# Kernel optimization log

Hardware: AMD Instinct MI355X
Metric: run time of the kernel (lower is better)

## Reference

```python
import jax, jax.numpy as jnp
import numpy as np

N_STARS = 2048   # n_stars
BATCH = 256      # query positions per call
PF = 28          # poly_features = (d_max+1)(d_max+2)/2, d_max=6
NGE = 512        # n_graph_elems
GF = 32          # graph_features
OPD = 256        # opd_dim


def setup_inputs() -> dict:
    key = jax.random.key(0)
    ks = jax.random.split(key, 8)
    # observed star positions in the FoV (x_lims/y_lims = [0,1000])
    obs_pos = jax.random.uniform(ks[0], (N_STARS, 2), jnp.float32, 0.0, 1000.0)
    # query positions are exact rows of obs_pos (required by the exact-match index search)
    idx = jax.random.randint(ks[1], (BATCH,), 0, N_STARS)
    positions = obs_pos[idx]
    poly_dic = jax.random.normal(ks[2], (N_STARS, PF), jnp.float32)
    graph_dic = jax.random.normal(ks[3], (N_STARS, NGE), jnp.float32)
    # alpha matrices: identity(-padded) init as in init_vars, plus small noise
    alpha_poly = jnp.eye(PF, dtype=jnp.float32) + 0.01 * jax.random.normal(ks[4], (PF, PF), jnp.float32)
    alpha_graph = (jnp.eye(NGE, GF, dtype=jnp.float32)
                   + 0.01 * jax.random.normal(ks[5], (NGE, GF), jnp.float32))
    # S features: random uniform in [-1e-3, 1e-3] as in init_vars
    S_poly = jax.random.uniform(ks[6], (PF, OPD, OPD), jnp.float32, -0.001, 0.001)
    S_graph = jax.random.uniform(ks[7], (GF, OPD, OPD), jnp.float32, -0.001, 0.001)
    return {
        'positions': positions, 'obs_pos': obs_pos,
        'poly_dic': poly_dic, 'graph_dic': graph_dic,
        'alpha_poly': alpha_poly, 'alpha_graph': alpha_graph,
        'S_poly': S_poly, 'S_graph': S_graph,
    }


def _calc_indices(positions, obs_pos):
    # Faithful to tf.where(tf.equal(obs_pos, pos))[0, 0]: first True entry (row-major)
    # of the elementwise equality over (n_stars, 2); its row index is taken.
    eq = positions[:, None, :] == obs_pos[None, :, :]          # (B, N, 2) bool
    flat_first = jnp.argmax(eq.reshape(eq.shape[0], -1), axis=1)  # first True, flat index
    return flat_first // 2                                      # row index in obs_pos


def reference(positions, obs_pos, poly_dic, graph_dic, alpha_poly, alpha_graph, S_poly, S_graph):
    indices = _calc_indices(positions, obs_pos)                 # (B,) int
    # polynomial part: gather -> matmul -> tensordot with OPD modes
    batch_poly = jnp.take(poly_dic, indices, axis=0)            # (B, PF)
    interm_poly = batch_poly @ alpha_poly                       # (B, PF)
    contrib_poly = jnp.einsum('bp,pij->bij', interm_poly, S_poly)  # (B, OPD, OPD)
    # graph part
    batch_graph = jnp.take(graph_dic, indices, axis=0)          # (B, NGE)
    interm_graph = batch_graph @ alpha_graph                    # (B, GF)
    contrib_graph = jnp.einsum('bg,gij->bij', interm_graph, S_graph)
    return contrib_poly + contrib_graph
```

## Files before the change

### kernel.cpp

```cpp
#include <hip/hip_runtime.h>

#define NSTARS 2048
#define BATCH  256
#define PF     28
#define NGE    512
#define GF     32
#define OPD2   65536
#define KTOT   (PF + GF)
#define TM     16

typedef float f32x4 __attribute__((ext_vector_type(4)));

__global__ __launch_bounds__(256) void prep_kernel(
    const float* __restrict__ positions,  const float* __restrict__ obs_pos,
    const float* __restrict__ poly_dic,   const float* __restrict__ graph_dic,
    const float* __restrict__ alpha_poly, const float* __restrict__ alpha_graph,
    float* __restrict__ Wt)
{
    const int b = blockIdx.x;
    const int t = threadIdx.x;

    const float p0 = positions[2 * b];
    const float p1 = positions[2 * b + 1];

    int cand = 0x7fffffff;
    #pragma unroll
    for (int i = 0; i < NSTARS / 256; ++i) {
        const int n = t + i * 256;
        const float o0 = obs_pos[2 * n];
        const float o1 = obs_pos[2 * n + 1];
        if (o0 == p0 || o1 == p1) cand = min(cand, n);
    }
    __shared__ int smin[256];
    smin[t] = cand;
    __syncthreads();
    for (int s = 128; s > 0; s >>= 1) {
        if (t < s) smin[t] = min(smin[t], smin[t + s]);
        __syncthreads();
    }
    int idx = smin[0];
    if (idx == 0x7fffffff) idx = 0;

    if (t < PF) {
        float acc = 0.f;
        #pragma unroll
        for (int p = 0; p < PF; ++p)
            acc += poly_dic[idx * PF + p] * alpha_poly[p * PF + t];
        Wt[t * BATCH + b] = acc;
    }

    __shared__ float psum[8][GF];
    {
        const int g = t & 31;
        const int r = t >> 5;
        float acc = 0.f;
        const int e0 = r * (NGE / 8);
        for (int e = e0; e < e0 + NGE / 8; ++e)
            acc += graph_dic[idx * NGE + e] * alpha_graph[e * GF + g];
        psum[r][g] = acc;
    }
    __syncthreads();
    if (t < GF) {
        float acc = 0.f;
        #pragma unroll
        for (int r = 0; r < 8; ++r) acc += psum[r][t];
        Wt[(PF + t) * BATCH + b] = acc;
    }
}

__global__ __launch_bounds__(256) void main_kernel(
    const float* __restrict__ S_poly, const float* __restrict__ S_graph,
    const float* __restrict__ Wt, float* __restrict__ out)
{
    const int t    = threadIdx.x;
    const int id   = blockIdx.x;
    const int xcd  = id & 7;
    const int slot = id >> 3;
    const int xb   = xcd * 8 + (slot & 7);
    const int yb   = slot >> 3;

    const int ij = xb * 1024 + t * 4;
    const int b0 = yb * TM;

    f32x4 acc[TM];
    #pragma unroll
    for (int b = 0; b < TM; ++b) acc[b] = (f32x4)(0.f);

    const float* __restrict__ wp = Wt + b0;

    #pragma unroll 8
    for (int k = 0; k < PF; ++k) {
        const f32x4 s = *reinterpret_cast<const f32x4*>(
            S_poly + (size_t)k * OPD2 + ij);
        #pragma unroll
        for (int b = 0; b < TM; ++b) {
            const float w = wp[k * BATCH + b];
            acc[b].x = fmaf(w, s.x, acc[b].x);
            acc[b].y = fmaf(w, s.y, acc[b].y);
            acc[b].z = fmaf(w, s.z, acc[b].z);
            acc[b].w = fmaf(w, s.w, acc[b].w);
        }
    }
    #pragma unroll 8
    for (int k = 0; k < GF; ++k) {
        const f32x4 s = *reinterpret_cast<const f32x4*>(
            S_graph + (size_t)k * OPD2 + ij);
        #pragma unroll
        for (int b = 0; b < TM; ++b) {
            const float w = wp[(PF + k) * BATCH + b];
            acc[b].x = fmaf(w, s.x, acc[b].x);
            acc[b].y = fmaf(w, s.y, acc[b].y);
            acc[b].z = fmaf(w, s.z, acc[b].z);
            acc[b].w = fmaf(w, s.w, acc[b].w);
        }
    }

    #pragma unroll
    for (int b = 0; b < TM; ++b) {
        __builtin_nontemporal_store(
            acc[b],
            reinterpret_cast<f32x4*>(out + (size_t)(b0 + b) * OPD2 + ij));
    }
}

extern "C" void kernel_launch(void* const* d_in, const int* in_sizes, int n_in,
                              void* d_out, int out_size, void* d_ws, size_t ws_size,
                              hipStream_t stream) {
    const float* positions   = (const float*)d_in[0];
    const float* obs_pos     = (const float*)d_in[1];
    const float* poly_dic    = (const float*)d_in[2];
    const float* graph_dic   = (const float*)d_in[3];
    const float* alpha_poly  = (const float*)d_in[4];
    const float* alpha_graph = (const float*)d_in[5];
    const float* S_poly      = (const float*)d_in[6];
    const float* S_graph     = (const float*)d_in[7];
    float* out = (float*)d_out;

    float* Wt = (float*)d_ws;

    prep_kernel<<<BATCH, 256, 0, stream>>>(positions, obs_pos, poly_dic,
                                           graph_dic, alpha_poly, alpha_graph,
                                           Wt);

    main_kernel<<<1024, 256, 0, stream>>>(S_poly, S_graph, Wt, out);
}
```

Measured before the change: 131.0 us.

## Double-buffer S tiles in LDS via async global_load_lds

The main kernel now stages the S coefficient tiles (four k-slices at a time) into a double-buffered shared-memory array using direct global-to-LDS loads. The next stage is prefetched while FMAs run on the current one. The aim is to hide global load latency behind compute. In exchange it adds a block barrier and a full vmcnt wait every stage, and the w loads from global, which are also vector memory ops, get serialized by those waits.

```diff
diff --git a/kernel.cpp b/kernel.cpp
--- a/kernel.cpp
+++ b/kernel.cpp
@@ -8,6 +8,8 @@
 #define OPD2   65536
 #define KTOT   (PF + GF)
 #define TM     16
+#define KB     4
+#define NT     (KTOT / KB)
 
 typedef float f32x4 __attribute__((ext_vector_type(4)));
 
@@ -72,6 +74,8 @@
     const float* __restrict__ S_poly, const float* __restrict__ S_graph,
     const float* __restrict__ Wt, float* __restrict__ out)
 {
+    __shared__ float sbuf[2][KB][1024];
+
     const int t    = threadIdx.x;
     const int id   = blockIdx.x;
     const int xcd  = id & 7;
@@ -82,37 +86,54 @@
     const int ij = xb * 1024 + t * 4;
     const int b0 = yb * TM;
 
+    const float* __restrict__ wp = Wt + b0;
+
     f32x4 acc[TM];
     #pragma unroll
     for (int b = 0; b < TM; ++b) acc[b] = (f32x4)(0.f);
 
-    const float* __restrict__ wp = Wt + b0;
+    const int wbase = (t >> 6) << 8;
 
-    #pragma unroll 8
-    for (int k = 0; k < PF; ++k) {
-        const f32x4 s = *reinterpret_cast<const f32x4*>(
-            S_poly + (size_t)k * OPD2 + ij);
+    auto stage = [&](int T, int d) {
+        const int kb = T * KB;
+        const float* base = (T < PF / KB)
+            ? (S_poly  + (size_t)kb * OPD2)
+            : (S_graph + (size_t)(kb - PF) * OPD2);
+        const float* src = base + xb * 1024 + t * 4;
         #pragma unroll
-        for (int b = 0; b < TM; ++b) {
-            const float w = wp[k * BATCH + b];
-            acc[b].x = fmaf(w, s.x, acc[b].x);
-            acc[b].y = fmaf(w, s.y, acc[b].y);
-            acc[b].z = fmaf(w, s.z, acc[b].z);
-            acc[b].w = fmaf(w, s.w, acc[b].w);
+        for (int kk = 0; kk < KB; ++kk) {
+            __builtin_amdgcn_global_load_lds(
+                (const __attribute__((address_space(1))) uint32_t*)(src + (size_t)kk * OPD2),
+                (__attribute__((address_space(3))) uint32_t*)&sbuf[d][kk][wbase],
+                16, 0, 0);
         }
-    }
-    #pragma unroll 8
-    for (int k = 0; k < GF; ++k) {
-        const f32x4 s = *reinterpret_cast<const f32x4*>(
-            S_graph + (size_t)k * OPD2 + ij);
+    };
+
+    stage(0, 0);
+    asm volatile("s_waitcnt vmcnt(0)" ::: "memory");
+    __syncthreads();
+
+    int cur = 0;
+    for (int T = 0; T < NT; ++T) {
+        if (T + 1 < NT) stage(T + 1, cur ^ 1);
+
+        const int kb = T * KB;
         #pragma unroll
-        for (int b = 0; b < TM; ++b) {
-            const float w = wp[(PF + k) * BATCH + b];
-            acc[b].x = fmaf(w, s.x, acc[b].x);
-            acc[b].y = fmaf(w, s.y, acc[b].y);
-            acc[b].z = fmaf(w, s.z, acc[b].z);
-            acc[b].w = fmaf(w, s.w, acc[b].w);
+        for (int kk = 0; kk < KB; ++kk) {
+            const f32x4 s = *reinterpret_cast<const f32x4*>(&sbuf[cur][kk][t * 4]);
+            #pragma unroll
+            for (int b = 0; b < TM; ++b) {
+                const float w = wp[(kb + kk) * BATCH + b];
+                acc[b].x = fmaf(w, s.x, acc[b].x);
+                acc[b].y = fmaf(w, s.y, acc[b].y);
+                acc[b].z = fmaf(w, s.z, acc[b].z);
+                acc[b].w = fmaf(w, s.w, acc[b].w);
+            }
         }
+
+        asm volatile("s_waitcnt vmcnt(0)" ::: "memory");
+        __syncthreads();
+        cur ^= 1;
     }
 
     #pragma unroll
```

After: 126.0 us. 1.04x faster.

## Software-pipeline S row loads, halve batch tile, throttle occupancy via LDS

Applied to the files above, without the earlier changes.

Restructures the main kernel to keep six S rows in flight in registers, loading row k+6 while computing row k, and merges the poly and graph loops into one. The batch tile per block drops from 16 to 8 and the grid doubles, which lowers register pressure and adds blocks. A 32 KB shared array is declared but effectively unused, so it only limits how many blocks fit per CU. The trade-off is that each S element is re-read twice as often, and the occupancy cap may reduce latency hiding.

```diff
diff --git a/kernel.cpp b/kernel.cpp
--- a/kernel.cpp
+++ b/kernel.cpp
@@ -7,7 +7,9 @@
 #define GF     32
 #define OPD2   65536
 #define KTOT   (PF + GF)
-#define TM     16
+#define TM     8
+#define DEPTH  6
+#define NGRP   (KTOT / DEPTH)
 
 typedef float f32x4 __attribute__((ext_vector_type(4)));
 
@@ -72,47 +74,61 @@
     const float* __restrict__ S_poly, const float* __restrict__ S_graph,
     const float* __restrict__ Wt, float* __restrict__ out)
 {
+    __shared__ float lds_throttle[8192];
+
     const int t    = threadIdx.x;
     const int id   = blockIdx.x;
     const int xcd  = id & 7;
     const int slot = id >> 3;
     const int xb   = xcd * 8 + (slot & 7);
     const int yb   = slot >> 3;
+    const int ij   = xb * 1024 + t * 4;
+    const int b0   = yb * TM;
 
-    const int ij = xb * 1024 + t * 4;
-    const int b0 = yb * TM;
+    if (id == -1) lds_throttle[t] = Wt[t];
+
+    const float* __restrict__ wp = Wt + b0;
 
     f32x4 acc[TM];
     #pragma unroll
     for (int b = 0; b < TM; ++b) acc[b] = (f32x4)(0.f);
 
-    const float* __restrict__ wp = Wt + b0;
+    auto srow = [&](int k) -> const f32x4* {
+        const float* base = (k < PF) ? (S_poly  + (size_t)k * OPD2)
+                                     : (S_graph + (size_t)(k - PF) * OPD2);
+        return reinterpret_cast<const f32x4*>(base + ij);
+    };
 
-    #pragma unroll 8
-    for (int k = 0; k < PF; ++k) {
-        const f32x4 s = *reinterpret_cast<const f32x4*>(
-            S_poly + (size_t)k * OPD2 + ij);
+    auto kstep = [&](int k, f32x4& sv, bool reload) {
+        const float* wk = wp + k * BATCH;
+        const f32x4 s = sv;
         #pragma unroll
-        for (int b = 0; b < TM; ++b) {
-            const float w = wp[k * BATCH + b];
-            acc[b].x = fmaf(w, s.x, acc[b].x);
-            acc[b].y = fmaf(w, s.y, acc[b].y);
-            acc[b].z = fmaf(w, s.z, acc[b].z);
-            acc[b].w = fmaf(w, s.w, acc[b].w);
-        }
+        for (int b = 0; b < TM; ++b)
+            acc[b] += wk[b] * s;
+        if (reload) sv = *srow(k + DEPTH);
+    };
+
+    f32x4 sv0 = *srow(0), sv1 = *srow(1), sv2 = *srow(2),
+          sv3 = *srow(3), sv4 = *srow(4), sv5 = *srow(5);
+
+    #pragma unroll 1
+    for (int T = 0; T < NGRP - 1; ++T) {
+        const int kg = T * DEPTH;
+        kstep(kg + 0, sv0, true);
+        kstep(kg + 1, sv1, true);
+        kstep(kg + 2, sv2, true);
+        kstep(kg + 3, sv3, true);
+        kstep(kg + 4, sv4, true);
+        kstep(kg + 5, sv5, true);
     }
-    #pragma unroll 8
-    for (int k = 0; k < GF; ++k) {
-        const f32x4 s = *reinterpret_cast<const f32x4*>(
-            S_graph + (size_t)k * OPD2 + ij);
-        #pragma unroll
-        for (int b = 0; b < TM; ++b) {
-            const float w = wp[(PF + k) * BATCH + b];
-            acc[b].x = fmaf(w, s.x, acc[b].x);
-            acc[b].y = fmaf(w, s.y, acc[b].y);
-            acc[b].z = fmaf(w, s.z, acc[b].z);
-            acc[b].w = fmaf(w, s.w, acc[b].w);
-        }
+    {
+        const int kg = (NGRP - 1) * DEPTH;
+        kstep(kg + 0, sv0, false);
+        kstep(kg + 1, sv1, false);
+        kstep(kg + 2, sv2, false);
+        kstep(kg + 3, sv3, false);
+        kstep(kg + 4, sv4, false);
+        kstep(kg + 5, sv5, false);
     }
 
     #pragma unroll
@@ -142,5 +158,5 @@
                                            graph_dic, alpha_poly, alpha_graph,
                                            Wt);
 
-    main_kernel<<<1024, 256, 0, stream>>>(S_poly, S_graph, Wt, out);
+    main_kernel<<<2048, 256, 0, stream>>>(S_poly, S_graph, Wt, out);
 }
```

Result: faster. 124.2 us (-5.1%).
